# Kernel optimization log

Hardware: AMD Instinct MI355X
Metric: run time of the kernel (lower is better)

Reference implementation:

```python
import jax, jax.numpy as jnp
import numpy as np

GRID_SIZE = 5
SPLINE_ORDER = 3
N_COEFF = GRID_SIZE + SPLINE_ORDER  # 8 basis functions per input feature
D_MODEL = 1024
D_FF = 4096


def make_grid(in_features):
    # uniform grid on [-1, 1] extended by spline_order knots each side
    h = 2.0 / GRID_SIZE
    g = np.arange(-SPLINE_ORDER, GRID_SIZE + SPLINE_ORDER + 1, dtype=np.float32) * h - 1.0
    return jnp.asarray(np.tile(g[None, :], (in_features, 1)))  # (in, G + 2k + 1)


def b_splines(x, grid):
    # x: (N, in) -> (N, in, G + k) via Cox-de Boor recursion
    xe = x[..., None]
    bases = ((xe >= grid[:, :-1]) & (xe < grid[:, 1:])).astype(x.dtype)
    for j in range(1, SPLINE_ORDER + 1):
        left = (xe - grid[:, : -(j + 1)]) / (grid[:, j:-1] - grid[:, : -(j + 1)])
        right = (grid[:, j + 1 :] - xe) / (grid[:, j + 1 :] - grid[:, 1:-j])
        bases = left * bases[..., :-1] + right * bases[..., 1:]
    return bases


def kan_linear(x, base_w, spline_w, grid):
    # x: (N, in); base_w: (out, in); spline_w: (out, in, C)
    base = jax.nn.silu(x) @ base_w.T
    b = b_splines(x, grid)                      # (N, in, C)
    spl = jnp.einsum('nic,oic->no', b, spline_w)
    return base + spl


def setup_inputs() -> dict:
    key = jax.random.key(0)
    ks = jax.random.split(key, 7)
    s_in = 1.0 / np.sqrt(D_MODEL)
    s_ff = 1.0 / np.sqrt(D_FF)
    return {
        'x': jax.random.normal(ks[0], (2, 2048, D_MODEL), jnp.float32),
        'base_w1': jax.random.normal(ks[1], (D_FF, D_MODEL), jnp.float32) * s_in,
        'spline_w1': jax.random.normal(ks[2], (D_FF, D_MODEL, N_COEFF), jnp.float32) * s_in * 0.1,
        'base_w2': jax.random.normal(ks[3], (D_FF, D_MODEL), jnp.float32) * s_in,
        'spline_w2': jax.random.normal(ks[4], (D_FF, D_MODEL, N_COEFF), jnp.float32) * s_in * 0.1,
        'base_w3': jax.random.normal(ks[5], (D_MODEL, D_FF), jnp.float32) * s_ff,
        'spline_w3': jax.random.normal(ks[6], (D_MODEL, D_FF, N_COEFF), jnp.float32) * s_ff * 0.1,
        'grid_in': make_grid(D_MODEL),
        'grid_ff': make_grid(D_FF),
    }


def reference(x, base_w1, spline_w1, base_w2, spline_w2, base_w3, spline_w3, grid_in, grid_ff):
    shp = x.shape
    x2 = x.reshape(-1, shp[-1])                      # (N, d_model)
    h = kan_linear(x2, base_w1, spline_w1, grid_in) * kan_linear(x2, base_w2, spline_w2, grid_in)
    out = kan_linear(h, base_w3, spline_w3, grid_ff)
    return out.reshape(shp)
```

## Files before the change

### kernel.cpp

```cpp
#include <hip/hip_runtime.h>
#include <hip/hip_bf16.h>
#include <cstdint>
#include <cstddef>
#include <type_traits>


#define D_MODEL 1024
#define D_FF    4096
#define NTOK    4096
#define NC      9
#define K1      (D_MODEL * NC)
#define K3      (D_FF * NC)
#define SPLITK2 16
#define SPLITKF 4
#define CHUNK   1024

typedef __attribute__((ext_vector_type(8))) short bf16x8;
typedef __attribute__((ext_vector_type(4))) float f32x4;

__device__ __forceinline__ unsigned short bf16b(float f) {
  __hip_bfloat16 h = __float2bfloat16(f);
  return __builtin_bit_cast(unsigned short, h);
}

__device__ __forceinline__ void kan_feat_u(float x, unsigned short* dst) {
  float s = x / (1.0f + __expf(-x));
  float B[11];
#pragma unroll
  for (int j = 0; j < 11; ++j) {
    float gj = -2.2f + 0.4f * j;
    B[j] = (x >= gj && x < gj + 0.4f) ? 1.0f : 0.0f;
  }
#pragma unroll
  for (int p = 1; p <= 3; ++p) {
    float inv = 1.0f / (0.4f * p);
#pragma unroll
    for (int i = 0; i + p < 11; ++i) {
      float gi = -2.2f + 0.4f * i;
      B[i] = (x - gi) * inv * B[i] + ((gi + 0.4f + 0.4f * p) - x) * inv * B[i + 1];
    }
  }
  dst[0] = bf16b(s);
#pragma unroll
  for (int c = 0; c < 8; ++c) dst[1 + c] = bf16b(B[c]);
}

__global__ void pack_kan_w(const float* __restrict__ bw, const float* __restrict__ sw,
                           __hip_bfloat16* __restrict__ W, int K, int inShift,
                           int rowMul, int rowBase, size_t totalPairs) {
  size_t t = (size_t)blockIdx.x * blockDim.x + threadIdx.x;
  if (t >= totalPairs) return;
  size_t o = t >> (inShift - 1);
  size_t ip = (t & (((size_t)1 << (inShift - 1)) - 1)) * 2;
  size_t e0 = (o << inShift) + ip;
  float2 b = *(const float2*)(bw + e0);
  const float4* sp = (const float4*)(sw + e0 * 8);
  float4 s0 = sp[0], s1 = sp[1], s2 = sp[2], s3 = sp[3];
  unsigned short h[18];
  h[0] = bf16b(b.x);
  h[1] = bf16b(s0.x); h[2] = bf16b(s0.y); h[3] = bf16b(s0.z); h[4] = bf16b(s0.w);
  h[5] = bf16b(s1.x); h[6] = bf16b(s1.y); h[7] = bf16b(s1.z); h[8] = bf16b(s1.w);
  h[9] = bf16b(b.y);
  h[10] = bf16b(s2.x); h[11] = bf16b(s2.y); h[12] = bf16b(s2.z); h[13] = bf16b(s2.w);
  h[14] = bf16b(s3.x); h[15] = bf16b(s3.y); h[16] = bf16b(s3.z); h[17] = bf16b(s3.w);
  uint32_t* dst = (uint32_t*)(W + (o * rowMul + rowBase) * (size_t)K + ip * NC);
#pragma unroll
  for (int k = 0; k < 9; ++k) dst[k] = (uint32_t)h[2 * k] | ((uint32_t)h[2 * k + 1] << 16);
}

__global__ void build_a1(const float* __restrict__ x, __hip_bfloat16* __restrict__ A1) {
  size_t t = (size_t)blockIdx.x * blockDim.x + threadIdx.x;
  if (t >= (size_t)NTOK * D_MODEL / 2) return;
  size_t n = t >> 9;
  size_t ip = (t & 511) * 2;
  float2 xv = *(const float2*)(x + n * D_MODEL + ip);
  unsigned short h[18];
  kan_feat_u(xv.x, h);
  kan_feat_u(xv.y, h + 9);
  uint32_t* dst = (uint32_t*)(A1 + n * (size_t)K1 + ip * NC);
#pragma unroll
  for (int k = 0; k < 9; ++k) dst[k] = (uint32_t)h[2 * k] | ((uint32_t)h[2 * k + 1] << 16);
}

template <typename HT>
__global__ void glu_a3(const HT* __restrict__ Hc, __hip_bfloat16* __restrict__ A3c) {
  size_t t = (size_t)blockIdx.x * blockDim.x + threadIdx.x;
  if (t >= (size_t)CHUNK * D_FF / 2) return;
  size_t n = t >> 11;
  size_t jp = (t & 2047) * 2;
  float a0, a1, c0, c1;
  if constexpr (std::is_same<HT, float>::value) {
    float2 u = *(const float2*)(Hc + n * 8192 + jp);
    float2 v = *(const float2*)(Hc + n * 8192 + 4096 + jp);
    a0 = u.x; a1 = u.y; c0 = v.x; c1 = v.y;
  } else {
    a0 = __bfloat162float(Hc[n * 8192 + jp]);
    a1 = __bfloat162float(Hc[n * 8192 + jp + 1]);
    c0 = __bfloat162float(Hc[n * 8192 + 4096 + jp]);
    c1 = __bfloat162float(Hc[n * 8192 + 4096 + jp + 1]);
  }
  unsigned short h[18];
  kan_feat_u(a0 * c0, h);
  kan_feat_u(a1 * c1, h + 9);
  uint32_t* dst = (uint32_t*)(A3c + n * (size_t)K3 + jp * NC);
#pragma unroll
  for (int k = 0; k < 9; ++k) dst[k] = (uint32_t)h[2 * k] | ((uint32_t)h[2 * k + 1] << 16);
}

#define STAGE(Ts)                                                                        \
  {                                                                                      \
    const int _sl = ((Ts) & 3) * 32768;                                                  \
    const size_t _ko = (size_t)(Ts) * 64;                                                \
    __builtin_amdgcn_global_load_lds(                                                    \
        (const __attribute__((address_space(1))) void*)(gA0 + _ko),                      \
        (__attribute__((address_space(3))) void*)(lds_raw + _sl + dA0), 16, 0, 0);       \
    __builtin_amdgcn_global_load_lds(                                                    \
        (const __attribute__((address_space(1))) void*)(gA1 + _ko),                      \
        (__attribute__((address_space(3))) void*)(lds_raw + _sl + dA1), 16, 0, 0);       \
    __builtin_amdgcn_global_load_lds(                                                    \
        (const __attribute__((address_space(1))) void*)(gB0 + _ko),                      \
        (__attribute__((address_space(3))) void*)(lds_raw + _sl + dB0), 16, 0, 0);       \
    __builtin_amdgcn_global_load_lds(                                                    \
        (const __attribute__((address_space(1))) void*)(gB1 + _ko),                      \
        (__attribute__((address_space(3))) void*)(lds_raw + _sl + dB1), 16, 0, 0);       \
  }

template <typename CT, bool FUSE>
__global__ __launch_bounds__(512, 2) void gemm256(
    const __hip_bfloat16* __restrict__ A, const __hip_bfloat16* __restrict__ Bw,
    CT* __restrict__ Cp, int N, int K, int kLen,
    __hip_bfloat16* __restrict__ A3out) {
  __shared__ __align__(16) char lds_raw[4 * 32768];

  const int tid = threadIdx.x;
  const int wid = tid >> 6, lane = tid & 63;
  const int wr = wid >> 2, wc = wid & 3;

  const int nwg = gridDim.x * gridDim.y;
  const int orig = blockIdx.y * gridDim.x + blockIdx.x;
  const int q = nwg >> 3, r = nwg & 7;
  const int xcd = orig & 7, lid = orig >> 3;
  const int wg = (xcd < r ? xcd * (q + 1) : r * (q + 1) + (xcd - r) * q) + lid;
  const int bx = wg % gridDim.x, by = wg / gridDim.x;

  const size_t brow = (size_t)by * 256;
  const size_t bcol = (size_t)bx * 256;
  const int kStart = (int)blockIdx.z * kLen;
  const int NT = kLen / 32;

  const int kbx = (lane & 3) ^ ((lane >> 3) & 3);
  const int rsub = lane >> 2;
  const char* gA0 = (const char*)A +
      ((brow + (size_t)(wid * 16 + rsub)) * (size_t)K + kStart + kbx * 8) * 2;
  const char* gA1 = (const char*)A +
      ((brow + 128 + (size_t)(wid * 16 + rsub)) * (size_t)K + kStart + kbx * 8) * 2;
  const char* gB0 = (const char*)Bw +
      ((bcol + (size_t)(wid * 16 + rsub)) * (size_t)K + kStart + kbx * 8) * 2;
  const char* gB1 = (const char*)Bw +
      ((bcol + 128 + (size_t)(wid * 16 + rsub)) * (size_t)K + kStart + kbx * 8) * 2;
  const int dA0 = wid * 1024;
  const int dA1 = 8192 + wid * 1024;
  const int dB0 = 16384 + wid * 1024;
  const int dB1 = 24576 + wid * 1024;

  const int fkb = (lane >> 4) ^ ((lane >> 1) & 3);
  const int aoff = (wr * 128 + (lane & 15)) * 64 + fkb * 16;
  const int boff = 16384 + (wc * 64 + (lane & 15)) * 64 + fkb * 16;

  f32x4 acc[8][4] = {};

  STAGE(0);
  STAGE(1);
  STAGE(2);
  asm volatile("s_waitcnt vmcnt(8)" ::: "memory");
  __builtin_amdgcn_s_barrier();

  for (int T = 0; T < NT; ++T) {
    if (T + 3 < NT) STAGE(T + 3);

    const int sl = (T & 3) * 32768;
    bf16x8 af[8], bfr[4];
#pragma unroll
    for (int mf = 0; mf < 8; ++mf)
      af[mf] = *(const bf16x8*)(lds_raw + sl + aoff + mf * 1024);
#pragma unroll
    for (int nf = 0; nf < 4; ++nf)
      bfr[nf] = *(const bf16x8*)(lds_raw + sl + boff + nf * 1024);

    __builtin_amdgcn_s_setprio(1);
#pragma unroll
    for (int mf = 0; mf < 8; ++mf)
#pragma unroll
      for (int nf = 0; nf < 4; ++nf)
        acc[mf][nf] =
            __builtin_amdgcn_mfma_f32_16x16x32_bf16(af[mf], bfr[nf], acc[mf][nf], 0, 0, 0);
    __builtin_amdgcn_s_setprio(0);

    if (T + 4 <= NT) {
      asm volatile("s_waitcnt vmcnt(8)" ::: "memory");
    } else if (T + 3 == NT) {
      asm volatile("s_waitcnt vmcnt(4)" ::: "memory");
    } else if (T + 2 == NT) {
      asm volatile("s_waitcnt vmcnt(0)" ::: "memory");
    }
    asm volatile("s_waitcnt lgkmcnt(0)" ::: "memory");
    __builtin_amdgcn_s_barrier();
  }

  if constexpr (FUSE) {
    float* gbuf = (float*)lds_raw;
#pragma unroll
    for (int mf = 0; mf < 8; ++mf) {
      const int s = wr * 8 + mf;
#pragma unroll
      for (int nf = 0; nf < 4; ++nf) {
#pragma unroll
        for (int rr = 0; rr < 4; ++rr) {
          float v = acc[mf][nf][rr];
          float w = __shfl_xor(v, 1, 64);
          if (!(lane & 1)) {
            const int r4 = (lane >> 4) * 4 + rr;
            const int ploc = wc * 32 + nf * 8 + ((lane & 14) >> 1);
            gbuf[s * 2048 + r4 * 128 + ploc] = v * w;
          }
        }
      }
    }
    __builtin_amdgcn_s_barrier();
    const int p2 = tid & 63;
    const int rb = tid >> 6;
    for (int k = 0; k < 32; ++k) {
      const int rr_ = rb + 8 * k;
      const int s = rr_ >> 4, rl = rr_ & 15;
      float g0 = gbuf[s * 2048 + rl * 128 + 2 * p2];
      float g1 = gbuf[s * 2048 + rl * 128 + 2 * p2 + 1];
      unsigned short h[18];
      kan_feat_u(g0, h);
      kan_feat_u(g1, h + 9);
      const size_t n = brow + rr_;
      const size_t pg = (bcol >> 1) + 2 * p2;
      uint32_t* dst = (uint32_t*)(A3out + n * (size_t)K3 + pg * NC);
#pragma unroll
      for (int qq = 0; qq < 9; ++qq)
        dst[qq] = (uint32_t)h[2 * qq] | ((uint32_t)h[2 * qq + 1] << 16);
    }
  } else {
#pragma unroll
    for (int mf = 0; mf < 8; ++mf)
#pragma unroll
      for (int nf = 0; nf < 4; ++nf) {
        const size_t r0 = brow + wr * 128 + mf * 16 + (lane >> 4) * 4;
        const size_t c0 = bcol + wc * 64 + nf * 16 + (lane & 15);
        const size_t M = (size_t)gridDim.y * 256;
        CT* C = Cp + (size_t)blockIdx.z * M * (size_t)N;
#pragma unroll
        for (int rr = 0; rr < 4; ++rr) {
          float v = acc[mf][nf][rr];
          if constexpr (std::is_same<CT, float>::value)
            C[(r0 + rr) * (size_t)N + c0] = v;
          else
            C[(r0 + rr) * (size_t)N + c0] = __float2bfloat16(v);
        }
      }
  }
}

__global__ void reduceK(const float* __restrict__ P, float* __restrict__ out,
                        size_t quarter, int nslice) {
  size_t t = (size_t)blockIdx.x * blockDim.x + threadIdx.x;
  if (t >= quarter) return;
  const float4* p = (const float4*)P;
  float4 a = p[t];
  for (int s = 1; s < nslice; ++s) {
    float4 b = p[(size_t)s * quarter + t];
    a.x += b.x; a.y += b.y; a.z += b.z; a.w += b.w;
  }
  ((float4*)out)[t] = a;
}

extern "C" void kernel_launch(void* const* d_in, const int* in_sizes, int n_in,
                              void* d_out, int out_size, void* d_ws, size_t ws_size,
                              hipStream_t stream) {
  const float* x   = (const float*)d_in[0];
  const float* bw1 = (const float*)d_in[1];
  const float* sw1 = (const float*)d_in[2];
  const float* bw2 = (const float*)d_in[3];
  const float* sw2 = (const float*)d_in[4];
  const float* bw3 = (const float*)d_in[5];
  const float* sw3 = (const float*)d_in[6];
  float* out = (float*)d_out;
  char* ws = (char*)d_ws;

  const size_t W12_B  = (size_t)8192 * K1 * 2;
  const size_t A1_B   = (size_t)NTOK * K1 * 2;
  const size_t A3F_B  = (size_t)NTOK * K3 * 2;
  const size_t A3C_B  = (size_t)CHUNK * K3 * 2;
  const size_t HF32_B = (size_t)NTOK * 8192 * 4;

  const bool fused = ws_size >= W12_B + A1_B + A3F_B;
  const bool hF32  = ws_size >= W12_B + A1_B + HF32_B;

  __hip_bfloat16* W12 = (__hip_bfloat16*)(ws);
  __hip_bfloat16* A1  = (__hip_bfloat16*)(ws + W12_B);
  __hip_bfloat16* W3  = A1;

  size_t pairs12 = (size_t)D_FF * D_MODEL / 2;
  int blocks12 = (int)((pairs12 + 255) / 256);
  size_t pairs3 = (size_t)D_MODEL * D_FF / 2;
  int blocks3 = (int)((pairs3 + 255) / 256);
  size_t pairsA1 = (size_t)NTOK * D_MODEL / 2;

  if (fused) {
    __hip_bfloat16* A3f = (__hip_bfloat16*)(ws + W12_B + A1_B);
    float*          Par = (float*)(ws);

    pack_kan_w<<<blocks12, 256, 0, stream>>>(bw1, sw1, W12, K1, 10, 2, 0, pairs12);
    pack_kan_w<<<blocks12, 256, 0, stream>>>(bw2, sw2, W12, K1, 10, 2, 1, pairs12);
    build_a1<<<(int)((pairsA1 + 255) / 256), 256, 0, stream>>>(x, A1);
    gemm256<float, true><<<dim3(8192 / 256, NTOK / 256, 1), 512, 0, stream>>>(
        A1, W12, nullptr, 8192, K1, K1, A3f);
    pack_kan_w<<<blocks3, 256, 0, stream>>>(bw3, sw3, W3, K3, 12, 1, 0, pairs3);
    gemm256<float, false><<<dim3(D_MODEL / 256, NTOK / 256, SPLITKF), 512, 0, stream>>>(
        A3f, W3, Par, D_MODEL, K3, K3 / SPLITKF, nullptr);
    size_t quarter = (size_t)NTOK * D_MODEL / 4;
    reduceK<<<(int)((quarter + 255) / 256), 256, 0, stream>>>(Par, out, quarter, SPLITKF);
  } else {
    void*           Hv  = (void*)(ws + W12_B + A1_B);
    __hip_bfloat16* A3c = (__hip_bfloat16*)(ws);
    float*          Par = (float*)(ws + A3C_B);

    pack_kan_w<<<blocks12, 256, 0, stream>>>(bw1, sw1, W12, K1, 10, 1, 0, pairs12);
    pack_kan_w<<<blocks12, 256, 0, stream>>>(bw2, sw2, W12, K1, 10, 1, 4096, pairs12);
    build_a1<<<(int)((pairsA1 + 255) / 256), 256, 0, stream>>>(x, A1);
    if (hF32)
      gemm256<float, false><<<dim3(8192 / 256, NTOK / 256, 1), 512, 0, stream>>>(
          A1, W12, (float*)Hv, 8192, K1, K1, nullptr);
    else
      gemm256<__hip_bfloat16, false><<<dim3(8192 / 256, NTOK / 256, 1), 512, 0, stream>>>(
          A1, W12, (__hip_bfloat16*)Hv, 8192, K1, K1, nullptr);
    pack_kan_w<<<blocks3, 256, 0, stream>>>(bw3, sw3, W3, K3, 12, 1, 0, pairs3);
    for (int c = 0; c < NTOK / CHUNK; ++c) {
      size_t pairsG = (size_t)CHUNK * D_FF / 2;
      int blocksG = (int)((pairsG + 255) / 256);
      if (hF32)
        glu_a3<float><<<blocksG, 256, 0, stream>>>(
            (const float*)Hv + (size_t)c * CHUNK * 8192, A3c);
      else
        glu_a3<__hip_bfloat16><<<blocksG, 256, 0, stream>>>(
            (const __hip_bfloat16*)Hv + (size_t)c * CHUNK * 8192, A3c);
      gemm256<float, false><<<dim3(D_MODEL / 256, CHUNK / 256, SPLITK2), 512, 0, stream>>>(
          A3c, W3, Par, D_MODEL, K3, K3 / SPLITK2, nullptr);
      size_t quarter = (size_t)CHUNK * D_MODEL / 4;
      reduceK<<<(int)((quarter + 255) / 256), 256, 0, stream>>>(
          Par, out + (size_t)c * CHUNK * D_MODEL, quarter, SPLITK2);
    }
  }
}
```

Before: 1.078 ms.

## Shrink GEMM tile to 256x128 with double-buffered LDS for higher occupancy

Halves the GEMM output tile width from 256 to 128 columns, cutting the per-block accumulators from 8x4 to 4x4 fragments and LDS from 128KB (4 stages) to 48KB (2 stages). Launch bounds are raised to allow 4 blocks per CU and the grids double in x. The pipeline moves the barrier to right after the fragment loads so the next stage can be issued earlier. The cost is less data reuse per block (A is reloaded twice as often) and a shallower prefetch depth, which may expose memory latency. The fused epilogue is remapped to the new tile shape.

```diff
diff --git a/kernel.cpp b/kernel.cpp
--- a/kernel.cpp
+++ b/kernel.cpp
@@ -14,6 +14,7 @@
 #define SPLITK2 16
 #define SPLITKF 4
 #define CHUNK   1024
+#define SLOT    24576
 
 typedef __attribute__((ext_vector_type(8))) short bf16x8;
 typedef __attribute__((ext_vector_type(4))) float f32x4;
@@ -109,7 +110,7 @@
 
 #define STAGE(Ts)                                                                        \
   {                                                                                      \
-    const int _sl = ((Ts) & 3) * 32768;                                                  \
+    const int _sl = ((Ts) & 1) * SLOT;                                                   \
     const size_t _ko = (size_t)(Ts) * 64;                                                \
     __builtin_amdgcn_global_load_lds(                                                    \
         (const __attribute__((address_space(1))) void*)(gA0 + _ko),                      \
@@ -120,21 +121,18 @@
     __builtin_amdgcn_global_load_lds(                                                    \
         (const __attribute__((address_space(1))) void*)(gB0 + _ko),                      \
         (__attribute__((address_space(3))) void*)(lds_raw + _sl + dB0), 16, 0, 0);       \
-    __builtin_amdgcn_global_load_lds(                                                    \
-        (const __attribute__((address_space(1))) void*)(gB1 + _ko),                      \
-        (__attribute__((address_space(3))) void*)(lds_raw + _sl + dB1), 16, 0, 0);       \
   }
 
 template <typename CT, bool FUSE>
-__global__ __launch_bounds__(512, 2) void gemm256(
+__global__ __launch_bounds__(512, 4) void gemm256(
     const __hip_bfloat16* __restrict__ A, const __hip_bfloat16* __restrict__ Bw,
     CT* __restrict__ Cp, int N, int K, int kLen,
     __hip_bfloat16* __restrict__ A3out) {
-  __shared__ __align__(16) char lds_raw[4 * 32768];
+  __shared__ __align__(16) char lds_raw[65536];
 
   const int tid = threadIdx.x;
   const int wid = tid >> 6, lane = tid & 63;
-  const int wr = wid >> 2, wc = wid & 3;
+  const int wr = wid >> 1, wc = wid & 1;
 
   const int nwg = gridDim.x * gridDim.y;
   const int orig = blockIdx.y * gridDim.x + blockIdx.x;
@@ -144,7 +142,7 @@
   const int bx = wg % gridDim.x, by = wg / gridDim.x;
 
   const size_t brow = (size_t)by * 256;
-  const size_t bcol = (size_t)bx * 256;
+  const size_t bcol = (size_t)bx * 128;
   const int kStart = (int)blockIdx.z * kLen;
   const int NT = kLen / 32;
 
@@ -156,62 +154,57 @@
       ((brow + 128 + (size_t)(wid * 16 + rsub)) * (size_t)K + kStart + kbx * 8) * 2;
   const char* gB0 = (const char*)Bw +
       ((bcol + (size_t)(wid * 16 + rsub)) * (size_t)K + kStart + kbx * 8) * 2;
-  const char* gB1 = (const char*)Bw +
-      ((bcol + 128 + (size_t)(wid * 16 + rsub)) * (size_t)K + kStart + kbx * 8) * 2;
   const int dA0 = wid * 1024;
   const int dA1 = 8192 + wid * 1024;
   const int dB0 = 16384 + wid * 1024;
-  const int dB1 = 24576 + wid * 1024;
 
   const int fkb = (lane >> 4) ^ ((lane >> 1) & 3);
-  const int aoff = (wr * 128 + (lane & 15)) * 64 + fkb * 16;
+  const int aoff = (wr * 64 + (lane & 15)) * 64 + fkb * 16;
   const int boff = 16384 + (wc * 64 + (lane & 15)) * 64 + fkb * 16;
 
-  f32x4 acc[8][4] = {};
+  f32x4 acc[4][4] = {};
 
   STAGE(0);
   STAGE(1);
-  STAGE(2);
-  asm volatile("s_waitcnt vmcnt(8)" ::: "memory");
+  asm volatile("s_waitcnt vmcnt(3)" ::: "memory");
   __builtin_amdgcn_s_barrier();
 
   for (int T = 0; T < NT; ++T) {
-    if (T + 3 < NT) STAGE(T + 3);
-
-    const int sl = (T & 3) * 32768;
-    bf16x8 af[8], bfr[4];
-#pragma unroll
-    for (int mf = 0; mf < 8; ++mf)
+    const int sl = (T & 1) * SLOT;
+    bf16x8 af[4], bfr[4];
+#pragma unroll
+    for (int mf = 0; mf < 4; ++mf)
       af[mf] = *(const bf16x8*)(lds_raw + sl + aoff + mf * 1024);
 #pragma unroll
     for (int nf = 0; nf < 4; ++nf)
       bfr[nf] = *(const bf16x8*)(lds_raw + sl + boff + nf * 1024);
+    asm volatile("s_waitcnt lgkmcnt(0)" ::: "memory");
+    __builtin_amdgcn_s_barrier();
+
+    if (T + 2 < NT) STAGE(T + 2);
 
     __builtin_amdgcn_s_setprio(1);
 #pragma unroll
-    for (int mf = 0; mf < 8; ++mf)
+    for (int mf = 0; mf < 4; ++mf)
 #pragma unroll
       for (int nf = 0; nf < 4; ++nf)
         acc[mf][nf] =
             __builtin_amdgcn_mfma_f32_16x16x32_bf16(af[mf], bfr[nf], acc[mf][nf], 0, 0, 0);
     __builtin_amdgcn_s_setprio(0);
 
-    if (T + 4 <= NT) {
-      asm volatile("s_waitcnt vmcnt(8)" ::: "memory");
-    } else if (T + 3 == NT) {
-      asm volatile("s_waitcnt vmcnt(4)" ::: "memory");
+    if (T + 2 < NT) {
+      asm volatile("s_waitcnt vmcnt(3)" ::: "memory");
     } else if (T + 2 == NT) {
       asm volatile("s_waitcnt vmcnt(0)" ::: "memory");
     }
-    asm volatile("s_waitcnt lgkmcnt(0)" ::: "memory");
     __builtin_amdgcn_s_barrier();
   }
 
   if constexpr (FUSE) {
     float* gbuf = (float*)lds_raw;
 #pragma unroll
-    for (int mf = 0; mf < 8; ++mf) {
-      const int s = wr * 8 + mf;
+    for (int mf = 0; mf < 4; ++mf) {
+      const int s = wr * 4 + mf;
 #pragma unroll
       for (int nf = 0; nf < 4; ++nf) {
 #pragma unroll
@@ -220,24 +213,22 @@
           float w = __shfl_xor(v, 1, 64);
           if (!(lane & 1)) {
             const int r4 = (lane >> 4) * 4 + rr;
-            const int ploc = wc * 32 + nf * 8 + ((lane & 14) >> 1);
-            gbuf[s * 2048 + r4 * 128 + ploc] = v * w;
+            const int p = wc * 32 + nf * 8 + ((lane & 14) >> 1);
+            gbuf[s * 1024 + r4 * 64 + p] = v * w;
           }
         }
       }
     }
     __builtin_amdgcn_s_barrier();
-    const int p2 = tid & 63;
-    const int rb = tid >> 6;
-    for (int k = 0; k < 32; ++k) {
-      const int rr_ = rb + 8 * k;
-      const int s = rr_ >> 4, rl = rr_ & 15;
-      float g0 = gbuf[s * 2048 + rl * 128 + 2 * p2];
-      float g1 = gbuf[s * 2048 + rl * 128 + 2 * p2 + 1];
+    const int p2 = tid & 31;
+    const int rb = tid >> 5;
+    for (int k = 0; k < 16; ++k) {
+      float2 g = *(const float2*)&gbuf[k * 1024 + rb * 64 + 2 * p2];
       unsigned short h[18];
-      kan_feat_u(g0, h);
-      kan_feat_u(g1, h + 9);
-      const size_t n = brow + rr_;
+      kan_feat_u(g.x, h);
+      kan_feat_u(g.y, h + 9);
+      const int row = (k >> 2) * 64 + (k & 3) * 16 + rb;
+      const size_t n = brow + row;
       const size_t pg = (bcol >> 1) + 2 * p2;
       uint32_t* dst = (uint32_t*)(A3out + n * (size_t)K3 + pg * NC);
 #pragma unroll
@@ -246,10 +237,10 @@
     }
   } else {
 #pragma unroll
-    for (int mf = 0; mf < 8; ++mf)
+    for (int mf = 0; mf < 4; ++mf)
 #pragma unroll
       for (int nf = 0; nf < 4; ++nf) {
-        const size_t r0 = brow + wr * 128 + mf * 16 + (lane >> 4) * 4;
+        const size_t r0 = brow + wr * 64 + mf * 16 + (lane >> 4) * 4;
         const size_t c0 = bcol + wc * 64 + nf * 16 + (lane & 15);
         const size_t M = (size_t)gridDim.y * 256;
         CT* C = Cp + (size_t)blockIdx.z * M * (size_t)N;
@@ -317,10 +308,10 @@
     pack_kan_w<<<blocks12, 256, 0, stream>>>(bw1, sw1, W12, K1, 10, 2, 0, pairs12);
     pack_kan_w<<<blocks12, 256, 0, stream>>>(bw2, sw2, W12, K1, 10, 2, 1, pairs12);
     build_a1<<<(int)((pairsA1 + 255) / 256), 256, 0, stream>>>(x, A1);
-    gemm256<float, true><<<dim3(8192 / 256, NTOK / 256, 1), 512, 0, stream>>>(
+    gemm256<float, true><<<dim3(8192 / 128, NTOK / 256, 1), 512, 0, stream>>>(
         A1, W12, nullptr, 8192, K1, K1, A3f);
     pack_kan_w<<<blocks3, 256, 0, stream>>>(bw3, sw3, W3, K3, 12, 1, 0, pairs3);
-    gemm256<float, false><<<dim3(D_MODEL / 256, NTOK / 256, SPLITKF), 512, 0, stream>>>(
+    gemm256<float, false><<<dim3(D_MODEL / 128, NTOK / 256, SPLITKF), 512, 0, stream>>>(
         A3f, W3, Par, D_MODEL, K3, K3 / SPLITKF, nullptr);
     size_t quarter = (size_t)NTOK * D_MODEL / 4;
     reduceK<<<(int)((quarter + 255) / 256), 256, 0, stream>>>(Par, out, quarter, SPLITKF);
@@ -333,10 +324,10 @@
     pack_kan_w<<<blocks12, 256, 0, stream>>>(bw2, sw2, W12, K1, 10, 1, 4096, pairs12);
     build_a1<<<(int)((pairsA1 + 255) / 256), 256, 0, stream>>>(x, A1);
     if (hF32)
-      gemm256<float, false><<<dim3(8192 / 256, NTOK / 256, 1), 512, 0, stream>>>(
+      gemm256<float, false><<<dim3(8192 / 128, NTOK / 256, 1), 512, 0, stream>>>(
           A1, W12, (float*)Hv, 8192, K1, K1, nullptr);
     else
-      gemm256<__hip_bfloat16, false><<<dim3(8192 / 256, NTOK / 256, 1), 512, 0, stream>>>(
+      gemm256<__hip_bfloat16, false><<<dim3(8192 / 128, NTOK / 256, 1), 512, 0, stream>>>(
           A1, W12, (__hip_bfloat16*)Hv, 8192, K1, K1, nullptr);
     pack_kan_w<<<blocks3, 256, 0, stream>>>(bw3, sw3, W3, K3, 12, 1, 0, pairs3);
     for (int c = 0; c < NTOK / CHUNK; ++c) {
@@ -348,7 +339,7 @@
       else
         glu_a3<__hip_bfloat16><<<blocksG, 256, 0, stream>>>(
             (const __hip_bfloat16*)Hv + (size_t)c * CHUNK * 8192, A3c);
-      gemm256<float, false><<<dim3(D_MODEL / 256, CHUNK / 256, SPLITK2), 512, 0, stream>>>(
+      gemm256<float, false><<<dim3(D_MODEL / 128, CHUNK / 256, SPLITK2), 512, 0, stream>>>(
           A3c, W3, Par, D_MODEL, K3, K3 / SPLITK2, nullptr);
       size_t quarter = (size_t)CHUNK * D_MODEL / 4;
       reduceK<<<(int)((quarter + 255) / 256), 256, 0, stream>>>(
```

New measurement: 1.203 ms. 11.6% more time.

## Switch GEMM mainloop to BK=64 double buffering with new swizzled LDS layout

Applied to the files above, without the earlier changes.

Changes the GEMM pipeline from a 4-deep ring of BK=32 stages to a 2-slot double buffer of BK=64 tiles. Each stage now issues eight 16-byte global-to-LDS loads per thread, uses an 8-way XOR swizzle over 128-byte rows, and runs two MFMA sub-steps per barrier. This halves the number of barriers and waitcnt points per K. In exchange the prefetch distance drops to one tile and every iteration waits on vmcnt(0), which may expose global load latency.

```diff
diff --git a/kernel.cpp b/kernel.cpp
--- a/kernel.cpp
+++ b/kernel.cpp
@@ -14,6 +14,7 @@
 #define SPLITK2 16
 #define SPLITKF 4
 #define CHUNK   1024
+#define SLOT    65536
 
 typedef __attribute__((ext_vector_type(8))) short bf16x8;
 typedef __attribute__((ext_vector_type(4))) float f32x4;
@@ -109,20 +110,19 @@
 
 #define STAGE(Ts)                                                                        \
   {                                                                                      \
-    const int _sl = ((Ts) & 3) * 32768;                                                  \
-    const size_t _ko = (size_t)(Ts) * 64;                                                \
-    __builtin_amdgcn_global_load_lds(                                                    \
-        (const __attribute__((address_space(1))) void*)(gA0 + _ko),                      \
-        (__attribute__((address_space(3))) void*)(lds_raw + _sl + dA0), 16, 0, 0);       \
-    __builtin_amdgcn_global_load_lds(                                                    \
-        (const __attribute__((address_space(1))) void*)(gA1 + _ko),                      \
-        (__attribute__((address_space(3))) void*)(lds_raw + _sl + dA1), 16, 0, 0);       \
-    __builtin_amdgcn_global_load_lds(                                                    \
-        (const __attribute__((address_space(1))) void*)(gB0 + _ko),                      \
-        (__attribute__((address_space(3))) void*)(lds_raw + _sl + dB0), 16, 0, 0);       \
-    __builtin_amdgcn_global_load_lds(                                                    \
-        (const __attribute__((address_space(1))) void*)(gB1 + _ko),                      \
-        (__attribute__((address_space(3))) void*)(lds_raw + _sl + dB1), 16, 0, 0);       \
+    const int _sl = ((Ts) & 1) * SLOT;                                                   \
+    const size_t _ko = (size_t)(Ts) * 128;                                               \
+    _Pragma("unroll") for (int _st = 0; _st < 4; ++_st) {                                \
+      __builtin_amdgcn_global_load_lds(                                                  \
+          (const __attribute__((address_space(1))) void*)(gA0 + _st * strideK + _ko),    \
+          (__attribute__((address_space(3))) void*)(lds_raw + _sl + _st * 8192 + dW),    \
+          16, 0, 0);                                                                     \
+      __builtin_amdgcn_global_load_lds(                                                  \
+          (const __attribute__((address_space(1))) void*)(gB0 + _st * strideK + _ko),    \
+          (__attribute__((address_space(3))) void*)(lds_raw + _sl + 32768 +              \
+                                                    _st * 8192 + dW),                    \
+          16, 0, 0);                                                                     \
+    }                                                                                    \
   }
 
 template <typename CT, bool FUSE>
@@ -130,7 +130,7 @@
     const __hip_bfloat16* __restrict__ A, const __hip_bfloat16* __restrict__ Bw,
     CT* __restrict__ Cp, int N, int K, int kLen,
     __hip_bfloat16* __restrict__ A3out) {
-  __shared__ __align__(16) char lds_raw[4 * 32768];
+  __shared__ __align__(16) char lds_raw[2 * SLOT];
 
   const int tid = threadIdx.x;
   const int wid = tid >> 6, lane = tid & 63;
@@ -146,47 +146,39 @@
   const size_t brow = (size_t)by * 256;
   const size_t bcol = (size_t)bx * 256;
   const int kStart = (int)blockIdx.z * kLen;
-  const int NT = kLen / 32;
-
-  const int kbx = (lane & 3) ^ ((lane >> 3) & 3);
-  const int rsub = lane >> 2;
+  const int NT = kLen / 64;
+
+  const int kbx = (lane & 7) ^ (lane >> 3);
+  const int rsub = lane >> 3;
+  const size_t strideK = (size_t)K * 128;
   const char* gA0 = (const char*)A +
-      ((brow + (size_t)(wid * 16 + rsub)) * (size_t)K + kStart + kbx * 8) * 2;
-  const char* gA1 = (const char*)A +
-      ((brow + 128 + (size_t)(wid * 16 + rsub)) * (size_t)K + kStart + kbx * 8) * 2;
+      ((brow + (size_t)(wid * 8 + rsub)) * (size_t)K + kStart + kbx * 8) * 2;
   const char* gB0 = (const char*)Bw +
-      ((bcol + (size_t)(wid * 16 + rsub)) * (size_t)K + kStart + kbx * 8) * 2;
-  const char* gB1 = (const char*)Bw +
-      ((bcol + 128 + (size_t)(wid * 16 + rsub)) * (size_t)K + kStart + kbx * 8) * 2;
-  const int dA0 = wid * 1024;
-  const int dA1 = 8192 + wid * 1024;
-  const int dB0 = 16384 + wid * 1024;
-  const int dB1 = 24576 + wid * 1024;
-
-  const int fkb = (lane >> 4) ^ ((lane >> 1) & 3);
-  const int aoff = (wr * 128 + (lane & 15)) * 64 + fkb * 16;
-  const int boff = 16384 + (wc * 64 + (lane & 15)) * 64 + fkb * 16;
+      ((bcol + (size_t)(wid * 8 + rsub)) * (size_t)K + kStart + kbx * 8) * 2;
+  const int dW = wid * 1024;
+
+  const int gx0 = (((lane >> 4) ^ (lane & 7))) * 16;
+  const int gx1 = ((((lane >> 4) + 4) ^ (lane & 7))) * 16;
+  const int arow = (wr * 128 + (lane & 15)) * 128;
+  const int brw = 32768 + (wc * 64 + (lane & 15)) * 128;
 
   f32x4 acc[8][4] = {};
 
   STAGE(0);
-  STAGE(1);
-  STAGE(2);
-  asm volatile("s_waitcnt vmcnt(8)" ::: "memory");
+  asm volatile("s_waitcnt vmcnt(0)" ::: "memory");
   __builtin_amdgcn_s_barrier();
 
   for (int T = 0; T < NT; ++T) {
-    if (T + 3 < NT) STAGE(T + 3);
-
-    const int sl = (T & 3) * 32768;
+    if (T + 1 < NT) STAGE(T + 1);
+
+    const int sl = (T & 1) * SLOT;
     bf16x8 af[8], bfr[4];
 #pragma unroll
     for (int mf = 0; mf < 8; ++mf)
-      af[mf] = *(const bf16x8*)(lds_raw + sl + aoff + mf * 1024);
+      af[mf] = *(const bf16x8*)(lds_raw + sl + arow + mf * 2048 + gx0);
 #pragma unroll
     for (int nf = 0; nf < 4; ++nf)
-      bfr[nf] = *(const bf16x8*)(lds_raw + sl + boff + nf * 1024);
-
+      bfr[nf] = *(const bf16x8*)(lds_raw + sl + brw + nf * 2048 + gx0);
     __builtin_amdgcn_s_setprio(1);
 #pragma unroll
     for (int mf = 0; mf < 8; ++mf)
@@ -195,14 +187,22 @@
         acc[mf][nf] =
             __builtin_amdgcn_mfma_f32_16x16x32_bf16(af[mf], bfr[nf], acc[mf][nf], 0, 0, 0);
     __builtin_amdgcn_s_setprio(0);
-
-    if (T + 4 <= NT) {
-      asm volatile("s_waitcnt vmcnt(8)" ::: "memory");
-    } else if (T + 3 == NT) {
-      asm volatile("s_waitcnt vmcnt(4)" ::: "memory");
-    } else if (T + 2 == NT) {
-      asm volatile("s_waitcnt vmcnt(0)" ::: "memory");
-    }
+#pragma unroll
+    for (int mf = 0; mf < 8; ++mf)
+      af[mf] = *(const bf16x8*)(lds_raw + sl + arow + mf * 2048 + gx1);
+#pragma unroll
+    for (int nf = 0; nf < 4; ++nf)
+      bfr[nf] = *(const bf16x8*)(lds_raw + sl + brw + nf * 2048 + gx1);
+    __builtin_amdgcn_s_setprio(1);
+#pragma unroll
+    for (int mf = 0; mf < 8; ++mf)
+#pragma unroll
+      for (int nf = 0; nf < 4; ++nf)
+        acc[mf][nf] =
+            __builtin_amdgcn_mfma_f32_16x16x32_bf16(af[mf], bfr[nf], acc[mf][nf], 0, 0, 0);
+    __builtin_amdgcn_s_setprio(0);
+
+    asm volatile("s_waitcnt vmcnt(0)" ::: "memory");
     asm volatile("s_waitcnt lgkmcnt(0)" ::: "memory");
     __builtin_amdgcn_s_barrier();
   }
```

Result: faster. 1.040 ms, median of 4 (-3.5%).
